# Performance work log

Hardware: AMD Instinct MI355X
Metric: run time of the kernel (lower is better)

Reference implementation:

```python
import jax, jax.numpy as jnp
import numpy as np

N = 100000
E = 1600000
IN_C, HID_C, OUT_C = 128, 128, 64


def setup_inputs() -> dict:
    key = jax.random.key(0)
    k_x, k_e, k_w1, k_w2 = jax.random.split(key, 4)
    x = jax.random.normal(k_x, (N, IN_C), dtype=jnp.float32)
    edge_index = jax.random.randint(k_e, (2, E), 0, N, dtype=jnp.int32)
    # nn.Linear default init: U(-1/sqrt(fan_in), 1/sqrt(fan_in)); bias init zeros per module
    lim1 = 1.0 / np.sqrt(IN_C)
    lim2 = 1.0 / np.sqrt(HID_C)
    W1 = jax.random.uniform(k_w1, (IN_C, HID_C), minval=-lim1, maxval=lim1, dtype=jnp.float32)
    b1 = jnp.zeros((HID_C,), dtype=jnp.float32)
    W2 = jax.random.uniform(k_w2, (HID_C, OUT_C), minval=-lim2, maxval=lim2, dtype=jnp.float32)
    b2 = jnp.zeros((OUT_C,), dtype=jnp.float32)
    return {"x": x, "edge_index": edge_index, "W1": W1, "b1": b1, "W2": W2, "b2": b2}


def _out_degree_gcn_conv(x, src, dst, W, b, n_nodes):
    # linear projection (no bias in lin)
    h = x @ W  # [N, out_c]
    # out-degree of each source node
    deg = jax.ops.segment_sum(jnp.ones((src.shape[0],), dtype=h.dtype), src, num_segments=n_nodes)
    deg_inv = 1.0 / jnp.maximum(deg, 1.0)  # clamp(min=1)
    h = h * deg_inv[:, None]
    # message: x_j = h[src]; aggregate: sum at dst
    out = jax.ops.segment_sum(h[src], dst, num_segments=n_nodes)  # [N, out_c]
    return out + b


def reference(x, edge_index, W1, b1, W2, b2):
    src, dst = edge_index[0], edge_index[1]
    n = x.shape[0]
    h = _out_degree_gcn_conv(x, src, dst, W1, b1, n)
    h = jax.nn.relu(h)
    # dropout p=0.0 -> identity
    out = _out_degree_gcn_conv(h, src, dst, W2, b2, n)
    return out
```

## Files before the change

### kernel.cpp

```cpp
#include <hip/hip_runtime.h>
#include <hip/hip_bf16.h>


typedef __attribute__((ext_vector_type(8))) short short8;
typedef __attribute__((ext_vector_type(4))) float floatx4;

__device__ inline unsigned short f2bf(float f) {
    union { float f; unsigned u; } v; v.f = f;
    return (unsigned short)((v.u + 0x8000u) >> 16);
}
__device__ inline float bf2f(unsigned b) {
    union { unsigned u; float f; } v; v.u = b << 16;
    return v.f;
}
__device__ inline float bf2f_hi(unsigned b) {
    union { unsigned u; float f; } v; v.u = b & 0xFFFF0000u;
    return v.f;
}

#define NBMAX 512
#define CAP   8192
#define CHUNK 8192

__global__ __launch_bounds__(256) void convw_kernel(
    const float* __restrict__ W1, const float* __restrict__ W2,
    unsigned short* __restrict__ Wb1, unsigned short* __restrict__ Wb2,
    int* __restrict__ cnt)
{
    int i = blockIdx.x * 256 + threadIdx.x;
    if (i < NBMAX * 32) cnt[i] = 0;
    if (i < 128 * 128) {
        int k = i >> 7, n = i & 127;
        Wb1[n * 128 + k] = f2bf(W1[k * 128 + n]);
    }
    i -= 128 * 128;
    if (i >= 0 && i < 128 * 64) {
        int k = i >> 6, n = i & 63;
        Wb2[n * 128 + k] = f2bf(W2[k * 64 + n]);
    }
}

__global__ __launch_bounds__(1024) void scatter2_kernel(
    const int* __restrict__ src, const int* __restrict__ dst, int E,
    int* __restrict__ cnt_d, int* __restrict__ cnt_s,
    unsigned* __restrict__ pairs, unsigned char* __restrict__ srcs_b, int NB,
    const float* __restrict__ x, unsigned short* __restrict__ xb, int NF8)
{
    const int EB = (E + CHUNK - 1) / CHUNK;
    const int t = threadIdx.x;
    const int bid = blockIdx.x;
    if (bid >= 2 * EB) {
        int i = (bid - 2 * EB) * 1024 + t;
        if (i < NF8) {
            float4 a0 = ((const float4*)x)[(size_t)i * 2];
            float4 a1 = ((const float4*)x)[(size_t)i * 2 + 1];
            uint4 st;
            st.x = (unsigned)f2bf(a0.x) | ((unsigned)f2bf(a0.y) << 16);
            st.y = (unsigned)f2bf(a0.z) | ((unsigned)f2bf(a0.w) << 16);
            st.z = (unsigned)f2bf(a1.x) | ((unsigned)f2bf(a1.y) << 16);
            st.w = (unsigned)f2bf(a1.z) | ((unsigned)f2bf(a1.w) << 16);
            ((uint4*)xb)[i] = st;
        }
        return;
    }
    __shared__ int hd[NBMAX], lb[NBMAX], bd[NBMAX], cd_[NBMAX];
    __shared__ unsigned staged[CHUNK];
    const bool phaseA = (bid < EB);
    const int c = phaseA ? bid : bid - EB;
    const int e0 = c * CHUNK;
    const int e1 = min(e0 + CHUNK, E);
    const int* __restrict__ key = phaseA ? dst : src;

    for (int i = t; i < NB; i += 1024) { hd[i] = 0; cd_[i] = 0; }
    __syncthreads();
    for (int i = e0 + t; i < e1; i += 1024)
        atomicAdd(&hd[key[i] >> 8], 1);
    __syncthreads();
    if (t < NBMAX) lb[t] = (t < NB) ? hd[t] : 0;
    __syncthreads();
    for (int o = 1; o < NBMAX; o <<= 1) {
        int add = (t >= o && t < NBMAX) ? lb[t - o] : 0;
        __syncthreads();
        if (t < NBMAX) lb[t] += add;
        __syncthreads();
    }
    int* __restrict__ gcnt = phaseA ? cnt_d : cnt_s;
    for (int i = t; i < NB; i += 1024)
        if (hd[i]) bd[i] = atomicAdd(&gcnt[i * 16], hd[i]);
    __syncthreads();

    const int wid = t >> 6, lane = t & 63;
    if (phaseA) {
        for (int i = e0 + t; i < e1; i += 1024) {
            int sv = src[i], dv = dst[i];
            int b = dv >> 8;
            int slot = atomicAdd(&cd_[b], 1);
            staged[lb[b] - hd[b] + slot] = ((unsigned)(dv & 255) << 24) | (unsigned)sv;
        }
        __syncthreads();
        for (int b = wid; b < NB; b += 16) {
            int len = hd[b];
            if (!len) continue;
            int start = lb[b] - len;
            size_t gbase = (size_t)b * CAP + bd[b];
            for (int j = lane; j < len; j += 64)
                pairs[gbase + j] = staged[start + j];
        }
    } else {
        unsigned char* stb = (unsigned char*)staged;
        for (int i = e0 + t; i < e1; i += 1024) {
            int sv = src[i];
            int b = sv >> 8;
            int slot = atomicAdd(&cd_[b], 1);
            stb[lb[b] - hd[b] + slot] = (unsigned char)(sv & 255);
        }
        __syncthreads();
        for (int b = wid; b < NB; b += 16) {
            int len = hd[b];
            if (!len) continue;
            int start = lb[b] - len;
            size_t gbase = (size_t)b * CAP + bd[b];
            for (int j = lane; j < len; j += 64)
                srcs_b[gbase + j] = stb[start + j];
        }
    }
}

__global__ __launch_bounds__(512) void bucket_finalize_kernel(
    const unsigned* __restrict__ pairs, const unsigned char* __restrict__ srcs_b,
    const int* __restrict__ cnt_d, const int* __restrict__ cnt_s,
    int* __restrict__ sorted_src, int2* __restrict__ se,
    float* __restrict__ deg_inv, int N)
{
    const int b = blockIdx.x;
    const int node0 = b << 8;
    const int t = threadIdx.x;
    const size_t base = (size_t)b * CAP;
    __shared__ int hist[256];
    __shared__ int cur[256];
    __shared__ int pre[256];

    const int cd = cnt_d[b * 16];
    if (t < 256) hist[t] = 0;
    __syncthreads();
    for (int i = t; i < cd; i += 512)
        atomicAdd(&hist[pairs[base + i] >> 24], 1);
    __syncthreads();
    int v = 0, v4 = 0;
    if (t < 256) {
        v = hist[t];
        v4 = (v + 3) & ~3;
        pre[t] = v4;
    }
    __syncthreads();
    for (int o = 1; o < 256; o <<= 1) {
        int add = (t >= o && t < 256) ? pre[t - o] : 0;
        __syncthreads();
        if (t < 256) pre[t] += add;
        __syncthreads();
    }
    if (t < 256) {
        int excl = pre[t] - v4;
        cur[t] = excl;
        if (node0 + t < N) {
            se[node0 + t] = make_int2((int)base + excl, (int)base + excl + v);
            for (int i = v; i < v4; ++i) sorted_src[base + excl + i] = N;
        }
    }
    __syncthreads();
    for (int i = t; i < cd; i += 512) {
        unsigned p = pairs[base + i];
        int pos = atomicAdd(&cur[p >> 24], 1);
        sorted_src[base + pos] = (int)(p & 0xFFFFFFu);
    }

    __syncthreads();
    if (t < 256) hist[t] = 0;
    __syncthreads();
    const int cs = cnt_s[b * 16];
    for (int i = t; i < cs; i += 512)
        atomicAdd(&hist[srcs_b[base + i]], 1);
    __syncthreads();
    if (t < 256 && node0 + t < N) {
        int d = hist[t];
        deg_inv[node0 + t] = 1.0f / (float)(d < 1 ? 1 : d);
    }
}

template <int NC, int SC>
__global__ __launch_bounds__(256) void gemm_mfma_kernel(
    const unsigned short* __restrict__ Ab, const unsigned short* __restrict__ Wb,
    const float* __restrict__ scale, unsigned short* __restrict__ Cb, int M)
{
    constexpr int NT = NC / 16;
    const int t = threadIdx.x;
    if (blockIdx.x == 0 && t < NC / 2)
        ((unsigned*)Cb)[(size_t)M * (NC / 2) + t] = 0;
    const int wm = t >> 6;
    const int lane = t & 63;
    const int lm = lane & 15;
    const int lk = (lane >> 4) * 8;

    const int r0 = blockIdx.x * 64 + wm * 16;
    int row = r0 + lm;
    if (row >= M) row = M - 1;

    floatx4 acc[NT];
#pragma unroll
    for (int j = 0; j < NT; ++j) acc[j] = (floatx4){0.f, 0.f, 0.f, 0.f};

#pragma unroll
    for (int kk = 0; kk < 4; ++kk) {
        const int kb = kk * 32 + lk;
        short8 af = *(const short8*)&Ab[(size_t)row * 128 + kb];
#pragma unroll
        for (int j = 0; j < NT; ++j) {
            short8 bfr = *(const short8*)&Wb[(size_t)(j * 16 + lm) * 128 + kb];
            acc[j] = __builtin_amdgcn_mfma_f32_16x16x32_bf16(af, bfr, acc[j], 0, 0, 0);
        }
    }

    const int rbase = r0 + (lane >> 4) * 4;
#pragma unroll
    for (int reg = 0; reg < 4; ++reg) {
        int rg = rbase + reg;
        if (rg < M) {
            float di = SC ? scale[rg] : 1.0f;
#pragma unroll
            for (int j = 0; j < NT; ++j)
                Cb[(size_t)rg * NC + j * 16 + lm] = f2bf(SC ? acc[j][reg] * di : acc[j][reg]);
        }
    }
}

#define LD128(vv, ii) uint2 vv = *(const uint2*)&val[(size_t)(ii) * 64 + 2 * l]
#define ACC8_128(I0, I1) do { \
    LD128(v0, I0.x); LD128(v1, I0.y); LD128(v2, I0.z); LD128(v3, I0.w); \
    LD128(v4, I1.x); LD128(v5, I1.y); LD128(v6, I1.z); LD128(v7, I1.w); \
    a0 += ((bf2f(v0.x & 0xFFFF) + bf2f(v1.x & 0xFFFF)) + (bf2f(v2.x & 0xFFFF) + bf2f(v3.x & 0xFFFF))) \
        + ((bf2f(v4.x & 0xFFFF) + bf2f(v5.x & 0xFFFF)) + (bf2f(v6.x & 0xFFFF) + bf2f(v7.x & 0xFFFF))); \
    a1 += ((bf2f_hi(v0.x) + bf2f_hi(v1.x)) + (bf2f_hi(v2.x) + bf2f_hi(v3.x))) \
        + ((bf2f_hi(v4.x) + bf2f_hi(v5.x)) + (bf2f_hi(v6.x) + bf2f_hi(v7.x))); \
    a2 += ((bf2f(v0.y & 0xFFFF) + bf2f(v1.y & 0xFFFF)) + (bf2f(v2.y & 0xFFFF) + bf2f(v3.y & 0xFFFF))) \
        + ((bf2f(v4.y & 0xFFFF) + bf2f(v5.y & 0xFFFF)) + (bf2f(v6.y & 0xFFFF) + bf2f(v7.y & 0xFFFF))); \
    a3 += ((bf2f_hi(v0.y) + bf2f_hi(v1.y)) + (bf2f_hi(v2.y) + bf2f_hi(v3.y))) \
        + ((bf2f_hi(v4.y) + bf2f_hi(v5.y)) + (bf2f_hi(v6.y) + bf2f_hi(v7.y))); \
} while (0)
#define ACC4_128(I0) do { \
    LD128(v0, I0.x); LD128(v1, I0.y); LD128(v2, I0.z); LD128(v3, I0.w); \
    a0 += (bf2f(v0.x & 0xFFFF) + bf2f(v1.x & 0xFFFF)) + (bf2f(v2.x & 0xFFFF) + bf2f(v3.x & 0xFFFF)); \
    a1 += (bf2f_hi(v0.x) + bf2f_hi(v1.x)) + (bf2f_hi(v2.x) + bf2f_hi(v3.x)); \
    a2 += (bf2f(v0.y & 0xFFFF) + bf2f(v1.y & 0xFFFF)) + (bf2f(v2.y & 0xFFFF) + bf2f(v3.y & 0xFFFF)); \
    a3 += (bf2f_hi(v0.y) + bf2f_hi(v1.y)) + (bf2f_hi(v2.y) + bf2f_hi(v3.y)); \
} while (0)

__global__ __launch_bounds__(256) void aggregate128_kernel(
    const int2* __restrict__ se, const int* __restrict__ sorted_src,
    const unsigned* __restrict__ val, const float* __restrict__ bias,
    const float* __restrict__ deg_inv, unsigned* __restrict__ outb, int N)
{
    int node = blockIdx.x * 8 + (threadIdx.x >> 5);
    if (node >= N) return;
    int l = threadIdx.x & 31;
    int2 r = se[node];
    int e = r.x;
    const int end4 = r.x + ((r.y - r.x + 3) & ~3);
    float a0 = 0.f, a1 = 0.f, a2 = 0.f, a3 = 0.f;

    if (e + 8 <= end4) {
        int4 i0 = *(const int4*)&sorted_src[e];
        int4 i1 = *(const int4*)&sorted_src[e + 4];
        for (; e + 16 <= end4; e += 8) {
            int4 n0 = *(const int4*)&sorted_src[e + 8];
            int4 n1 = *(const int4*)&sorted_src[e + 12];
            ACC8_128(i0, i1);
            i0 = n0; i1 = n1;
        }
        ACC8_128(i0, i1);
        e += 8;
    }
    if (e < end4) {
        int4 i0 = *(const int4*)&sorted_src[e];
        ACC4_128(i0);
    }

    float di = deg_inv[node];
    float4 bv = *(const float4*)&bias[4 * l];
    a0 = fmaxf(a0 + bv.x, 0.f) * di;
    a1 = fmaxf(a1 + bv.y, 0.f) * di;
    a2 = fmaxf(a2 + bv.z, 0.f) * di;
    a3 = fmaxf(a3 + bv.w, 0.f) * di;
    uint2 o;
    o.x = (unsigned)f2bf(a0) | ((unsigned)f2bf(a1) << 16);
    o.y = (unsigned)f2bf(a2) | ((unsigned)f2bf(a3) << 16);
    *(uint2*)&outb[(size_t)node * 64 + 2 * l] = o;
}

#define LD64(vv, ii) unsigned vv = val[(size_t)(ii) * 32 + l]
#define ACC8_64(I0, I1) do { \
    LD64(v0, I0.x); LD64(v1, I0.y); LD64(v2, I0.z); LD64(v3, I0.w); \
    LD64(v4, I1.x); LD64(v5, I1.y); LD64(v6, I1.z); LD64(v7, I1.w); \
    ax += ((bf2f(v0 & 0xFFFF) + bf2f(v1 & 0xFFFF)) + (bf2f(v2 & 0xFFFF) + bf2f(v3 & 0xFFFF))) \
        + ((bf2f(v4 & 0xFFFF) + bf2f(v5 & 0xFFFF)) + (bf2f(v6 & 0xFFFF) + bf2f(v7 & 0xFFFF))); \
    ay += ((bf2f_hi(v0) + bf2f_hi(v1)) + (bf2f_hi(v2) + bf2f_hi(v3))) \
        + ((bf2f_hi(v4) + bf2f_hi(v5)) + (bf2f_hi(v6) + bf2f_hi(v7))); \
} while (0)
#define ACC4_64(I0) do { \
    LD64(v0, I0.x); LD64(v1, I0.y); LD64(v2, I0.z); LD64(v3, I0.w); \
    ax += (bf2f(v0 & 0xFFFF) + bf2f(v1 & 0xFFFF)) + (bf2f(v2 & 0xFFFF) + bf2f(v3 & 0xFFFF)); \
    ay += (bf2f_hi(v0) + bf2f_hi(v1)) + (bf2f_hi(v2) + bf2f_hi(v3)); \
} while (0)

__global__ __launch_bounds__(256) void aggregate64_kernel(
    const int2* __restrict__ se, const int* __restrict__ sorted_src,
    const unsigned* __restrict__ val, const float* __restrict__ bias,
    float* __restrict__ out, int N)
{
    int node = blockIdx.x * 8 + (threadIdx.x >> 5);
    if (node >= N) return;
    int l = threadIdx.x & 31;
    int2 r = se[node];
    int e = r.x;
    const int end4 = r.x + ((r.y - r.x + 3) & ~3);
    float ax = 0.f, ay = 0.f;

    if (e + 8 <= end4) {
        int4 i0 = *(const int4*)&sorted_src[e];
        int4 i1 = *(const int4*)&sorted_src[e + 4];
        for (; e + 16 <= end4; e += 8) {
            int4 n0 = *(const int4*)&sorted_src[e + 8];
            int4 n1 = *(const int4*)&sorted_src[e + 12];
            ACC8_64(i0, i1);
            i0 = n0; i1 = n1;
        }
        ACC8_64(i0, i1);
        e += 8;
    }
    if (e < end4) {
        int4 i0 = *(const int4*)&sorted_src[e];
        ACC4_64(i0);
    }

    float2 o = make_float2(ax + bias[2 * l], ay + bias[2 * l + 1]);
    *(float2*)&out[(size_t)node * 64 + 2 * l] = o;
}

extern "C" void kernel_launch(void* const* d_in, const int* in_sizes, int n_in,
                              void* d_out, int out_size, void* d_ws, size_t ws_size,
                              hipStream_t stream) {
    const float* x  = (const float*)d_in[0];
    const int*   ei = (const int*)d_in[1];
    const float* W1 = (const float*)d_in[2];
    const float* b1 = (const float*)d_in[3];
    const float* W2 = (const float*)d_in[4];
    const float* b2 = (const float*)d_in[5];
    float* out = (float*)d_out;

    const int N = in_sizes[0] / 128;
    const int E = in_sizes[1] / 2;
    const int* src = ei;
    const int* dst = ei + E;
    const int NB = (N + 255) >> 8;

    char* ws = (char*)d_ws;
    size_t off = 0;
    auto alloc = [&](size_t bytes) {
        void* p = ws + off;
        off = (off + bytes + 255) & ~(size_t)255;
        return p;
    };
    float* deg_inv  = (float*)alloc((size_t)N * 4);
    int2*  se       = (int2*)alloc((size_t)N * 8);
    int*   cnt_d    = (int*)alloc((size_t)NBMAX * 16 * 4 * 2);
    int*   cnt_s    = cnt_d + (size_t)NBMAX * 16;
    unsigned short* Wb1 = (unsigned short*)alloc((size_t)128 * 128 * 2);
    unsigned short* Wb2 = (unsigned short*)alloc((size_t)64 * 128 * 2);
    unsigned*      pairs  = (unsigned*)alloc((size_t)NBMAX * CAP * 4);
    unsigned char* srcs_b = (unsigned char*)alloc((size_t)NBMAX * CAP);
    int*   sorted_src = (int*)alloc((size_t)NBMAX * CAP * 4);
    unsigned short* h    = (unsigned short*)alloc((size_t)(N + 1) * 128 * 2);
    unsigned short* out1 = (unsigned short*)alloc((size_t)N * 128 * 2);
    unsigned short* xb = out1;
    unsigned short* g = ((size_t)(N + 1) * 128 <= (size_t)NBMAX * CAP * 4)
                            ? (unsigned short*)pairs
                            : (unsigned short*)alloc((size_t)(N + 1) * 64 * 2);

    convw_kernel<<<96, 256, 0, stream>>>(W1, W2, Wb1, Wb2, cnt_d);

    const int EB = (E + CHUNK - 1) / CHUNK;
    const int NF8 = (N * 128) / 8;
    const int CB = (NF8 + 1023) / 1024;
    scatter2_kernel<<<2 * EB + CB, 1024, 0, stream>>>(src, dst, E, cnt_d, cnt_s,
                                                      pairs, srcs_b, NB, x, xb, NF8);
    bucket_finalize_kernel<<<NB, 512, 0, stream>>>(pairs, srcs_b, cnt_d, cnt_s,
                                                   sorted_src, se, deg_inv, N);

    const int gblocks = (N + 63) / 64;
    const int ablocks = (N + 7) / 8;
    gemm_mfma_kernel<128, 1><<<gblocks, 256, 0, stream>>>(xb, Wb1, deg_inv, h, N);
    aggregate128_kernel<<<ablocks, 256, 0, stream>>>(se, sorted_src, (const unsigned*)h, b1,
                                                     deg_inv, (unsigned*)out1, N);
    gemm_mfma_kernel<64, 0><<<gblocks, 256, 0, stream>>>(out1, Wb2, nullptr, g, N);
    aggregate64_kernel<<<ablocks, 256, 0, stream>>>(se, sorted_src, (const unsigned*)g, b2, out, N);
}
```

Measured before the change: 277.8 us.

## Fuse layer-1 aggregation with layer-2 GEMM through an LDS tile

```diff
diff --git a/kernel.cpp b/kernel.cpp
--- a/kernel.cpp
+++ b/kernel.cpp
@@ -187,12 +187,11 @@
     }
 }
 
-template <int NC, int SC>
 __global__ __launch_bounds__(256) void gemm_mfma_kernel(
     const unsigned short* __restrict__ Ab, const unsigned short* __restrict__ Wb,
     const float* __restrict__ scale, unsigned short* __restrict__ Cb, int M)
 {
-    constexpr int NT = NC / 16;
+    constexpr int NC = 128, NT = NC / 16;
     const int t = threadIdx.x;
     if (blockIdx.x == 0 && t < NC / 2)
         ((unsigned*)Cb)[(size_t)M * (NC / 2) + t] = 0;
@@ -225,10 +224,10 @@
     for (int reg = 0; reg < 4; ++reg) {
         int rg = rbase + reg;
         if (rg < M) {
-            float di = SC ? scale[rg] : 1.0f;
+            float di = scale[rg];
 #pragma unroll
             for (int j = 0; j < NT; ++j)
-                Cb[(size_t)rg * NC + j * 16 + lm] = f2bf(SC ? acc[j][reg] * di : acc[j][reg]);
+                Cb[(size_t)rg * NC + j * 16 + lm] = f2bf(acc[j][reg] * di);
         }
     }
 }
@@ -254,46 +253,80 @@
     a3 += (bf2f_hi(v0.y) + bf2f_hi(v1.y)) + (bf2f_hi(v2.y) + bf2f_hi(v3.y)); \
 } while (0)
 
-__global__ __launch_bounds__(256) void aggregate128_kernel(
+__global__ __launch_bounds__(256) void agg128_gemm_kernel(
     const int2* __restrict__ se, const int* __restrict__ sorted_src,
     const unsigned* __restrict__ val, const float* __restrict__ bias,
-    const float* __restrict__ deg_inv, unsigned* __restrict__ outb, int N)
-{
-    int node = blockIdx.x * 8 + (threadIdx.x >> 5);
-    if (node >= N) return;
-    int l = threadIdx.x & 31;
-    int2 r = se[node];
-    int e = r.x;
-    const int end4 = r.x + ((r.y - r.x + 3) & ~3);
+    const float* __restrict__ deg_inv, const unsigned short* __restrict__ Wb2,
+    unsigned short* __restrict__ g, int N)
+{
+    __shared__ unsigned short tile[16 * 128];
+    const int t = threadIdx.x;
+    ((unsigned*)tile)[512 + t] = 0;
+    ((unsigned*)tile)[768 + t] = 0;
+    if (blockIdx.x == 0 && t < 32) ((unsigned*)g)[(size_t)N * 32 + t] = 0;
+
+    const int hw = t >> 5;
+    const int l = t & 31;
+    const int node = blockIdx.x * 8 + hw;
     float a0 = 0.f, a1 = 0.f, a2 = 0.f, a3 = 0.f;
-
-    if (e + 8 <= end4) {
-        int4 i0 = *(const int4*)&sorted_src[e];
-        int4 i1 = *(const int4*)&sorted_src[e + 4];
-        for (; e + 16 <= end4; e += 8) {
-            int4 n0 = *(const int4*)&sorted_src[e + 8];
-            int4 n1 = *(const int4*)&sorted_src[e + 12];
+    if (node < N) {
+        int2 r = se[node];
+        int e = r.x;
+        const int end4 = r.x + ((r.y - r.x + 3) & ~3);
+        if (e + 8 <= end4) {
+            int4 i0 = *(const int4*)&sorted_src[e];
+            int4 i1 = *(const int4*)&sorted_src[e + 4];
+            for (; e + 16 <= end4; e += 8) {
+                int4 n0 = *(const int4*)&sorted_src[e + 8];
+                int4 n1 = *(const int4*)&sorted_src[e + 12];
+                ACC8_128(i0, i1);
+                i0 = n0; i1 = n1;
+            }
             ACC8_128(i0, i1);
-            i0 = n0; i1 = n1;
-        }
-        ACC8_128(i0, i1);
-        e += 8;
-    }
-    if (e < end4) {
-        int4 i0 = *(const int4*)&sorted_src[e];
-        ACC4_128(i0);
-    }
-
-    float di = deg_inv[node];
-    float4 bv = *(const float4*)&bias[4 * l];
-    a0 = fmaxf(a0 + bv.x, 0.f) * di;
-    a1 = fmaxf(a1 + bv.y, 0.f) * di;
-    a2 = fmaxf(a2 + bv.z, 0.f) * di;
-    a3 = fmaxf(a3 + bv.w, 0.f) * di;
-    uint2 o;
-    o.x = (unsigned)f2bf(a0) | ((unsigned)f2bf(a1) << 16);
-    o.y = (unsigned)f2bf(a2) | ((unsigned)f2bf(a3) << 16);
-    *(uint2*)&outb[(size_t)node * 64 + 2 * l] = o;
+            e += 8;
+        }
+        if (e < end4) {
+            int4 i0 = *(const int4*)&sorted_src[e];
+            ACC4_128(i0);
+        }
+        float di = deg_inv[node];
+        float4 bv = *(const float4*)&bias[4 * l];
+        a0 = fmaxf(a0 + bv.x, 0.f) * di;
+        a1 = fmaxf(a1 + bv.y, 0.f) * di;
+        a2 = fmaxf(a2 + bv.z, 0.f) * di;
+        a3 = fmaxf(a3 + bv.w, 0.f) * di;
+    }
+    {
+        unsigned w0 = (unsigned)f2bf(a0) | ((unsigned)f2bf(a1) << 16);
+        unsigned w1 = (unsigned)f2bf(a2) | ((unsigned)f2bf(a3) << 16);
+        unsigned* p = (unsigned*)&tile[hw * 128 + ((((l >> 1) ^ hw) & 15) << 3) + (l & 1) * 4];
+        p[0] = w0;
+        p[1] = w1;
+    }
+    __syncthreads();
+
+    const int w = t >> 6;
+    const int lane = t & 63;
+    const int lm = lane & 15;
+    const int lk = (lane >> 4) * 8;
+    floatx4 acc = (floatx4){0.f, 0.f, 0.f, 0.f};
+#pragma unroll
+    for (int kk = 0; kk < 4; ++kk) {
+        const int kb = kk * 32 + lk;
+        const int blk = ((kb >> 3) ^ (lm & 7)) & 15;
+        short8 af = *(const short8*)&tile[lm * 128 + (blk << 3)];
+        short8 bfr = *(const short8*)&Wb2[(size_t)(w * 16 + lm) * 128 + kb];
+        acc = __builtin_amdgcn_mfma_f32_16x16x32_bf16(af, bfr, acc, 0, 0, 0);
+    }
+    const int rbase = (lane >> 4) * 4;
+#pragma unroll
+    for (int reg = 0; reg < 4; ++reg) {
+        int r = rbase + reg;
+        if (r < 8) {
+            int nd = blockIdx.x * 8 + r;
+            if (nd < N) g[(size_t)nd * 64 + w * 16 + lm] = f2bf(acc[reg]);
+        }
+    }
 }
 
 #define LD64(vv, ii) unsigned vv = val[(size_t)(ii) * 32 + l]
@@ -378,9 +411,8 @@
     unsigned*      pairs  = (unsigned*)alloc((size_t)NBMAX * CAP * 4);
     unsigned char* srcs_b = (unsigned char*)alloc((size_t)NBMAX * CAP);
     int*   sorted_src = (int*)alloc((size_t)NBMAX * CAP * 4);
-    unsigned short* h    = (unsigned short*)alloc((size_t)(N + 1) * 128 * 2);
-    unsigned short* out1 = (unsigned short*)alloc((size_t)N * 128 * 2);
-    unsigned short* xb = out1;
+    unsigned short* h  = (unsigned short*)alloc((size_t)(N + 1) * 128 * 2);
+    unsigned short* xb = (unsigned short*)alloc((size_t)N * 128 * 2);
     unsigned short* g = ((size_t)(N + 1) * 128 <= (size_t)NBMAX * CAP * 4)
                             ? (unsigned short*)pairs
                             : (unsigned short*)alloc((size_t)(N + 1) * 64 * 2);
@@ -397,9 +429,8 @@
 
     const int gblocks = (N + 63) / 64;
     const int ablocks = (N + 7) / 8;
-    gemm_mfma_kernel<128, 1><<<gblocks, 256, 0, stream>>>(xb, Wb1, deg_inv, h, N);
-    aggregate128_kernel<<<ablocks, 256, 0, stream>>>(se, sorted_src, (const unsigned*)h, b1,
-                                                     deg_inv, (unsigned*)out1, N);
-    gemm_mfma_kernel<64, 0><<<gblocks, 256, 0, stream>>>(out1, Wb2, nullptr, g, N);
+    gemm_mfma_kernel<<<gblocks, 256, 0, stream>>>(xb, Wb1, deg_inv, h, N);
+    agg128_gemm_kernel<<<ablocks, 256, 0, stream>>>(se, sorted_src, (const unsigned*)h, b1,
+                                                    deg_inv, Wb2, g, N);
     aggregate64_kernel<<<ablocks, 256, 0, stream>>>(se, sorted_src, (const unsigned*)g, b2, out, N);
 }
```

Result: faster. 271.5 us (-2.3%).
